# Kernel optimization log

Measured on AMD Instinct MI355X. Metric: run time of the kernel, lower is better.

## Reference

```python
import jax, jax.numpy as jnp
import numpy as np

B, S, HID = 1, 4096, 2048
HQ, HKV, D = 16, 8, 128
G = HQ // HKV
WINDOW = 1024
EPS = 1e-6
ROPE_THETA = 1e6


def setup_inputs() -> dict:
    key = jax.random.key(0)
    ks = jax.random.split(key, 6)
    hidden_states = jax.random.normal(ks[0], (B, S, HID), dtype=jnp.float32)
    Wq = jax.random.normal(ks[1], (HQ * D, HID), dtype=jnp.float32) * 0.02
    Wk = jax.random.normal(ks[2], (HKV * D, HID), dtype=jnp.float32) * 0.02
    Wv = jax.random.normal(ks[3], (HKV * D, HID), dtype=jnp.float32) * 0.02
    Wo = jax.random.normal(ks[4], (HID, HQ * D), dtype=jnp.float32) * 0.02
    q_norm_w = jnp.ones((D,), dtype=jnp.float32)
    k_norm_w = jnp.ones((D,), dtype=jnp.float32)
    # standard RoPE tables
    inv_freq = 1.0 / (ROPE_THETA ** (jnp.arange(0, D, 2, dtype=jnp.float32) / D))
    pos = jnp.arange(S, dtype=jnp.float32)
    freqs = pos[:, None] * inv_freq[None, :]            # [S, D/2]
    emb = jnp.concatenate([freqs, freqs], axis=-1)       # [S, D]
    cos = jnp.cos(emb)[None]                             # [1, S, D]
    sin = jnp.sin(emb)[None]
    return {"hidden_states": hidden_states, "cos": cos, "sin": sin,
            "Wq": Wq, "Wk": Wk, "Wv": Wv, "Wo": Wo,
            "q_norm_w": q_norm_w, "k_norm_w": k_norm_w}


def _rms_norm(x, w):
    var = jnp.mean(jnp.square(x), axis=-1, keepdims=True)
    return w * (x * jax.lax.rsqrt(var + EPS))


def _rotate_half(x):
    x1, x2 = jnp.split(x, 2, axis=-1)
    return jnp.concatenate([-x2, x1], axis=-1)


def reference(hidden_states, cos, sin, Wq, Wk, Wv, Wo, q_norm_w, k_norm_w):
    b, s, _ = hidden_states.shape
    # projections -> [B, H, S, D]
    q = (hidden_states @ Wq.T).reshape(b, s, HQ, D)
    k = (hidden_states @ Wk.T).reshape(b, s, HKV, D)
    v = (hidden_states @ Wv.T).reshape(b, s, HKV, D)
    q = _rms_norm(q, q_norm_w).transpose(0, 2, 1, 3)   # [B,HQ,S,D]
    k = _rms_norm(k, k_norm_w).transpose(0, 2, 1, 3)   # [B,HKV,S,D]
    v = v.transpose(0, 2, 1, 3)
    # RoPE (cos/sin broadcast over head dim)
    c = cos[:, None, :, :]
    sn = sin[:, None, :, :]
    q = q * c + _rotate_half(q) * sn
    k = k * c + _rotate_half(k) * sn
    # GQA: group queries per kv head
    qg = q.reshape(b, HKV, G, s, D)
    scaling = D ** -0.5
    scores = jnp.einsum('bhgqd,bhkd->bhgqk', qg, k) * scaling  # [B,HKV,G,S,S]
    # causal + sliding-window additive mask
    i = jnp.arange(s)[:, None]
    j = jnp.arange(s)[None, :]
    allowed = (j <= i) & (j > i - WINDOW)
    scores = jnp.where(allowed[None, None, None], scores, jnp.float32(-1e9))
    attn = jax.nn.softmax(scores, axis=-1)
    out = jnp.einsum('bhgqk,bhkd->bhgqd', attn, v)     # [B,HKV,G,S,D]
    out = out.reshape(b, HQ, s, D).transpose(0, 2, 1, 3).reshape(b, s, HQ * D)
    return out @ Wo.T
```

## Files before the change

### kernel.cpp

```cpp
#include <hip/hip_runtime.h>

typedef __bf16 bf16;
typedef bf16 bf16x8 __attribute__((ext_vector_type(8)));
typedef bf16 bf16x4 __attribute__((ext_vector_type(4)));
typedef float f32x4 __attribute__((ext_vector_type(4)));

#define MFMA16(a, b, c) __builtin_amdgcn_mfma_f32_16x16x32_bf16((a), (b), (c), 0, 0, 0)

__device__ __forceinline__ void gload_lds16(const bf16* g, bf16* l) {
  __builtin_amdgcn_global_load_lds(
      (const __attribute__((address_space(1))) void*)g,
      (__attribute__((address_space(3))) void*)l, 16, 0, 0);
}

template <int N>
__device__ __forceinline__ void lgkm_fence() {
  if constexpr (N == 0) asm volatile("s_waitcnt lgkmcnt(0)" ::: "memory");
  else if constexpr (N == 4) asm volatile("s_waitcnt lgkmcnt(4)" ::: "memory");
  else if constexpr (N == 8) asm volatile("s_waitcnt lgkmcnt(8)" ::: "memory");
  else if constexpr (N == 12) asm volatile("s_waitcnt lgkmcnt(12)" ::: "memory");
  __builtin_amdgcn_sched_barrier(0);
}
__device__ __forceinline__ void bar_fence() {
  __builtin_amdgcn_sched_barrier(0);
  __builtin_amdgcn_s_barrier();
}

__global__ __launch_bounds__(256) void cvt_f32_bf16(const float* __restrict__ src,
                                                    bf16* __restrict__ dst, int n4) {
  int i = blockIdx.x * blockDim.x + threadIdx.x;
  if (i < n4) {
    float4 v = ((const float4*)src)[i];
    bf16x4 o;
    o[0] = (bf16)v.x; o[1] = (bf16)v.y; o[2] = (bf16)v.z; o[3] = (bf16)v.w;
    ((bf16x4*)dst)[i] = o;
  }
}

template <int BM, int BN, int MT, int NTT, typename OutT>
__global__ __launch_bounds__(512, 2) void gemm_pipe(const bf16* __restrict__ A,
                                                    const bf16* __restrict__ B,
                                                    OutT* __restrict__ C,
                                                    int M, int N, int K) {
  constexpr int MH = MT / 2, NH = NTT / 2;
  constexpr int ASLOT = BM * 64;
  constexpr int BSLOT = BN * 64;
  constexpr int NLA = BM / 64, NLB = BN / 64;
  __shared__ __align__(16) bf16 SA[2 * ASLOT];
  __shared__ __align__(16) bf16 SB[2 * BSLOT];

  const int NTILES = K >> 6;
  const int tid = threadIdx.x;
  const int w = tid >> 6, lane = tid & 63;
  const int l15 = lane & 15, quad = lane >> 4;
  const int wr = w >> 2, wc = w & 3;

  const int nbx = N / BN;
  const int nwg = (M / BM) * nbx;
  const int wg = ((int)blockIdx.x & 7) * (nwg >> 3) + ((int)blockIdx.x >> 3);
  const int bm0 = (wg / nbx) * BM;
  const int bn0 = (wg % nbx) * BN;

  const int r0 = tid >> 3;
  const int sg = (tid & 7) ^ ((tid >> 3) & 7);
  unsigned aoffg[NLA], boffg[NLB];
#pragma unroll
  for (int i = 0; i < NLA; ++i)
    aoffg[i] = (unsigned)((bm0 + r0 + i * 64) * K + sg * 8);
#pragma unroll
  for (int i = 0; i < NLB; ++i)
    boffg[i] = (unsigned)((bn0 + r0 + i * 64) * K + sg * 8);

  const int xl = l15 & 7;
  const int p0 = quad ^ xl;
  const int baseA0 = (wr * (MT * 16) + l15) * 128 + p0 * 16;
  const int baseA1 = (wr * (MT * 16) + l15) * 128 + ((p0 ^ 4) * 16);
  const int baseB0 = (wc * (NTT * 16) + l15) * 128 + p0 * 16;
  const int baseB1 = (wc * (NTT * 16) + l15) * 128 + ((p0 ^ 4) * 16);
  const char* saB = (const char*)&SA[0];
  const char* sbB = (const char*)&SB[0];

  f32x4 acc[MT][NTT] = {};
  bf16x8 As[2][MH][2];
  bf16x8 Bs[2][NH][2];

#define LDA_(SL, H, DST)                                                        \
  _Pragma("unroll") for (int mt = 0; mt < MH; ++mt) {                           \
    (DST)[mt][0] = *(const bf16x8*)(saB + (SL) * (ASLOT * 2) + baseA0 +         \
                                    ((H) * MH + mt) * 2048);                    \
    (DST)[mt][1] = *(const bf16x8*)(saB + (SL) * (ASLOT * 2) + baseA1 +         \
                                    ((H) * MH + mt) * 2048);                    \
  }
#define LDB_(SL, G, DST)                                                        \
  _Pragma("unroll") for (int nt = 0; nt < NH; ++nt) {                           \
    (DST)[nt][0] = *(const bf16x8*)(sbB + (SL) * (BSLOT * 2) + baseB0 +         \
                                    ((G) * NH + nt) * 2048);                    \
    (DST)[nt][1] = *(const bf16x8*)(sbB + (SL) * (BSLOT * 2) + baseB1 +         \
                                    ((G) * NH + nt) * 2048);                    \
  }
#define QMFMA_(AS, BS, MHI, NHI)                                                \
  __builtin_amdgcn_s_setprio(1);                                                \
  _Pragma("unroll") for (int mt = 0; mt < MH; ++mt)                             \
      _Pragma("unroll") for (int nt = 0; nt < NH; ++nt) {                       \
    acc[(MHI) * MH + mt][(NHI) * NH + nt] = MFMA16(                             \
        (AS)[mt][0], (BS)[nt][0], acc[(MHI) * MH + mt][(NHI) * NH + nt]);       \
    acc[(MHI) * MH + mt][(NHI) * NH + nt] = MFMA16(                             \
        (AS)[mt][1], (BS)[nt][1], acc[(MHI) * MH + mt][(NHI) * NH + nt]);       \
  }                                                                             \
  __builtin_amdgcn_s_setprio(0);
#define STAGE_(SO, TS)                                                          \
  _Pragma("unroll") for (int i = 0; i < NLA; ++i)                               \
      gload_lds16(A + aoffg[i] + (TS) * 64, SA + (SO) * ASLOT + tid * 8 + i * 4096); \
  _Pragma("unroll") for (int i = 0; i < NLB; ++i)                               \
      gload_lds16(B + boffg[i] + (TS) * 64, SB + (SO) * BSLOT + tid * 8 + i * 4096);

#define GTILE_BODY(PAR, TS)                                                     \
  {                                                                             \
    constexpr int sl_ = (PAR), so_ = (PAR) ^ 1;                                 \
    constexpr int e0_ = (PAR), e1_ = (PAR) ^ 1;                                 \
                                                                        \
    LDB_(sl_, 1, Bs[e1_]);                                                      \
    bar_fence();                                                                \
    lgkm_fence<NTT>();                                                          \
    if ((TS) < NTILES) { STAGE_(so_, (TS)); }                                   \
    QMFMA_(As[0], Bs[e0_], 0, 0);                                               \
                                                                        \
    LDA_(sl_, 1, As[1]);                                                        \
    bar_fence();                                                                \
    lgkm_fence<MT>();                                                           \
    QMFMA_(As[0], Bs[e1_], 0, 1);                                               \
                                                                        \
    LDB_(sl_, 0, Bs[e0_]);                                                      \
    asm volatile("s_waitcnt vmcnt(0)" ::: "memory");                            \
    bar_fence();                                                                \
    lgkm_fence<NTT>();                                                          \
    QMFMA_(As[1], Bs[e1_], 1, 1);                                               \
                                                                        \
    LDA_(so_, 0, As[0]);                                                        \
    LDB_(so_, 0, Bs[e1_]);                                                      \
    bar_fence();                                                                \
    lgkm_fence<MT + NTT>();                                                     \
    QMFMA_(As[1], Bs[e0_], 1, 0);                                               \
  }

  { STAGE_(0, 0); }
  asm volatile("s_waitcnt vmcnt(0)" ::: "memory");
  bar_fence();
  __builtin_amdgcn_sched_barrier(0);
  LDA_(0, 0, As[0]);
  LDB_(0, 0, Bs[0]);

  for (int t = 0; t < NTILES; t += 2) {
    GTILE_BODY(0, t + 1);
    GTILE_BODY(1, t + 2);
  }

#undef LDA_
#undef LDB_
#undef QMFMA_
#undef STAGE_
#undef GTILE_BODY

#pragma unroll
  for (int mt = 0; mt < MT; ++mt)
#pragma unroll
    for (int nt = 0; nt < NTT; ++nt) {
      int row = bm0 + wr * (MT * 16) + mt * 16 + quad * 4;
      int col = bn0 + wc * (NTT * 16) + nt * 16 + l15;
#pragma unroll
      for (int r = 0; r < 4; ++r)
        C[(size_t)(row + r) * N + col] = (OutT)acc[mt][nt][r];
    }
}

__global__ __launch_bounds__(256) void normrope(const bf16* __restrict__ QKVb,
                                                const float* __restrict__ cosb,
                                                const float* __restrict__ sinb,
                                                const float* __restrict__ qw,
                                                const float* __restrict__ kw,
                                                bf16* __restrict__ Qb,
                                                bf16* __restrict__ Kb) {
  const int wid = (blockIdx.x * blockDim.x + threadIdx.x) >> 6;
  const int lane = threadIdx.x & 63;
  const int s = wid / 24;
  const int h = wid % 24;
  const bool isq = (h < 16);
  const int col0 = isq ? h * 128 : 2048 + (h - 16) * 128;
  const float* wt = isq ? qw : kw;

  const bf16* row = QKVb + (size_t)s * 4096 + col0;
  float x1 = (float)row[lane];
  float x2 = (float)row[lane + 64];

  float ss = x1 * x1 + x2 * x2;
#pragma unroll
  for (int m = 32; m >= 1; m >>= 1) ss += __shfl_xor(ss, m, 64);
  float rs = rsqrtf(ss * (1.0f / 128.0f) + 1e-6f);

  float c = cosb[(size_t)s * 128 + lane];
  float sn = sinb[(size_t)s * 128 + lane];
  float xn1 = x1 * rs * wt[lane];
  float xn2 = x2 * rs * wt[lane + 64];
  float o1 = xn1 * c - xn2 * sn;
  float o2 = xn2 * c + xn1 * sn;
  const float scale = isq ? 0.12751652f : 1.0f;
  o1 *= scale; o2 *= scale;

  bf16* dst = isq ? (Qb + ((size_t)h * 4096 + s) * 128)
                  : (Kb + ((size_t)(h - 16) * 4096 + s) * 128);
  dst[lane] = (bf16)o1;
  dst[lane + 64] = (bf16)o2;
}

__global__ __launch_bounds__(256) void vtrans(const bf16* __restrict__ QKVb,
                                              bf16* __restrict__ Vtp) {
  __shared__ __align__(16) bf16 T[64 * 136];
  const int kvh = blockIdx.y;
  const int s0 = blockIdx.x * 64;
  const int tid = threadIdx.x;
  for (int g = tid; g < 1024; g += 256) {
    int s = g >> 4, cg = g & 15;
    *(bf16x8*)(T + s * 136 + cg * 8) =
        *(const bf16x8*)(QKVb + (size_t)(s0 + s) * 4096 + 3072 + kvh * 128 + cg * 8);
  }
  __syncthreads();
  for (int g = tid; g < 1024; g += 256) {
    int d = g >> 3, sg = g & 7;
    bf16x8 v;
#pragma unroll
    for (int j = 0; j < 8; j++) {
      int kp = sg * 8 + j;
      int s = (kp & 3) * 16 + (kp >> 2);
      v[j] = T[s * 136 + d];
    }
    *(bf16x8*)(Vtp + ((size_t)kvh * 128 + d) * 4096 + s0 + sg * 8) = v;
  }
}

__global__ __launch_bounds__(512, 1) void attn_kernel(const bf16* __restrict__ Qb,
                                                      const bf16* __restrict__ Kb,
                                                      const bf16* __restrict__ Vtp,
                                                      bf16* __restrict__ Ob) {
  const int SEQ = 4096, W = 1024;
  const float MP = 17.312340f;
  __shared__ __align__(16) bf16 Ks[2][64 * 128];
  __shared__ __align__(16) bf16 Vs[2][128 * 64];
  __shared__ __align__(16) bf16 Ps[8][32 * 64];

  const int id = blockIdx.x;
  const int kvh = id & 7, gq = (id >> 3) & 1, h = kvh * 2 + gq;
  const int qb0 = (id >> 4) * 256;
  const int tid = threadIdx.x, w = tid >> 6, lane = tid & 63;
  const int l15 = lane & 15, quad = lane >> 4;
  const int qw0 = qb0 + w * 32;

  bf16x8 qf[2][4];
#pragma unroll
  for (int m = 0; m < 2; m++) {
    const bf16* qp = Qb + ((size_t)h * SEQ + qw0 + m * 16 + l15) * 128 + quad * 8;
#pragma unroll
    for (int kb = 0; kb < 4; kb++) qf[m][kb] = *(const bf16x8*)(qp + kb * 32);
  }

  f32x4 o[2][8] = {};
  f32x4 lr[2] = {};
  bf16* pw = &Ps[w][0];
  const bf16* kbase = Kb + (size_t)kvh * SEQ * 128;
  const bf16* vbase = Vtp + (size_t)kvh * 128 * SEQ;

  int jmin = qb0 - (W - 1); if (jmin < 0) jmin = 0;
  const int kt0 = jmin >> 6, kt1 = (qb0 + 255) >> 6;

#define ASTAGE(KT, SL)                                                          \
  do {                                                                          \
    const int k0_ = (KT) * 64;                                                  \
    _Pragma("unroll") for (int i_ = 0; i_ < 2; ++i_) {                          \
      int slot = i_ * 512 + tid;                                                \
      int key = slot >> 4, gg = slot & 15;                                      \
      int gsw = gg ^ (key & 7);                                                 \
      gload_lds16(kbase + (size_t)(k0_ + key) * 128 + gsw * 8,                  \
                  &Ks[SL][0] + slot * 8);                                       \
    }                                                                           \
    _Pragma("unroll") for (int i_ = 0; i_ < 2; ++i_) {                          \
      int slot = i_ * 512 + tid;                                                \
      int d = slot >> 3, gg = slot & 7;                                         \
      int gsw = gg ^ (d & 7);                                                   \
      gload_lds16(vbase + (size_t)d * SEQ + k0_ + gsw * 8,                      \
                  &Vs[SL][0] + slot * 8);                                       \
    }                                                                           \
  } while (0)

  ASTAGE(kt0, 0);

  for (int kt = kt0; kt <= kt1; ++kt) {
    const int sl = (kt - kt0) & 1;
    if (kt < kt1) {
      ASTAGE(kt + 1, sl ^ 1);
      asm volatile("s_waitcnt vmcnt(4)" ::: "memory");
    } else {
      asm volatile("s_waitcnt vmcnt(0)" ::: "memory");
    }
    __builtin_amdgcn_s_barrier();

    const int k0 = kt * 64;
    const bf16* ks = &Ks[sl][0];
    const bf16* vs = &Vs[sl][0];
    const bool alive = (k0 <= qw0 + 31) && (k0 + 63 > qw0 - W);
    if (alive) {
      const bool full = (k0 + 63 <= qw0) && (k0 > qw0 + 31 - W);
      f32x4 s[2][4] = {};
#pragma unroll
      for (int c = 0; c < 4; c++) {
        const int key = c * 16 + l15;
        bf16x8 kf[4];
#pragma unroll
        for (int kb = 0; kb < 4; kb++)
          kf[kb] = *(const bf16x8*)(ks + key * 128 + (((kb * 4 + quad) ^ (key & 7)) << 3));
        __builtin_amdgcn_s_setprio(1);
#pragma unroll
        for (int kb = 0; kb < 4; kb++) {
          s[0][c] = MFMA16(qf[0][kb], kf[kb], s[0][c]);
          s[1][c] = MFMA16(qf[1][kb], kf[kb], s[1][c]);
        }
        __builtin_amdgcn_s_setprio(0);
      }
#pragma unroll
      for (int m = 0; m < 2; m++)
#pragma unroll
        for (int r = 0; r < 4; r++) {
          float p[4];
          if (full) {
#pragma unroll
            for (int c = 0; c < 4; c++) p[c] = __builtin_amdgcn_exp2f(s[m][c][r] - MP);
          } else {
            const int i_ = qw0 + m * 16 + quad * 4 + r;
#pragma unroll
            for (int c = 0; c < 4; c++) {
              int j = k0 + c * 16 + l15;
              p[c] = (j <= i_ && j > i_ - W) ? __builtin_amdgcn_exp2f(s[m][c][r] - MP) : 0.0f;
            }
          }
          lr[m][r] += p[0] + p[1] + p[2] + p[3];
          bf16x4 pk;
          pk[0] = (bf16)p[0]; pk[1] = (bf16)p[1]; pk[2] = (bf16)p[2]; pk[3] = (bf16)p[3];
          const int qrow = m * 16 + quad * 4 + r;
          *(bf16x4*)(pw + qrow * 64 + (((l15 >> 1) ^ (qrow & 7)) << 3) + (l15 & 1) * 4) = pk;
        }
      asm volatile("s_waitcnt lgkmcnt(0)" ::: "memory");
      bf16x8 pf[2][2];
#pragma unroll
      for (int m = 0; m < 2; m++)
#pragma unroll
        for (int kb = 0; kb < 2; kb++)
          pf[m][kb] = *(const bf16x8*)(pw + (m * 16 + l15) * 64 +
                                       (((kb * 4 + quad) ^ (l15 & 7)) << 3));
#pragma unroll
      for (int n = 0; n < 8; n++) {
        const int d = n * 16 + l15;
        bf16x8 vf0 = *(const bf16x8*)(vs + d * 64 + ((quad ^ (l15 & 7)) << 3));
        bf16x8 vf1 = *(const bf16x8*)(vs + d * 64 + (((4 + quad) ^ (l15 & 7)) << 3));
        __builtin_amdgcn_s_setprio(1);
        o[0][n] = MFMA16(pf[0][0], vf0, o[0][n]);
        o[0][n] = MFMA16(pf[0][1], vf1, o[0][n]);
        o[1][n] = MFMA16(pf[1][0], vf0, o[1][n]);
        o[1][n] = MFMA16(pf[1][1], vf1, o[1][n]);
        __builtin_amdgcn_s_setprio(0);
      }
    }
    __builtin_amdgcn_s_barrier();
  }
#undef ASTAGE

  float linv[2][4];
#pragma unroll
  for (int m = 0; m < 2; m++)
#pragma unroll
    for (int r = 0; r < 4; r++) {
      float v = lr[m][r];
      v += __shfl_xor(v, 1, 64);
      v += __shfl_xor(v, 2, 64);
      v += __shfl_xor(v, 4, 64);
      v += __shfl_xor(v, 8, 64);
      linv[m][r] = 1.0f / v;
    }
#pragma unroll
  for (int m = 0; m < 2; m++)
#pragma unroll
    for (int n = 0; n < 8; n++)
#pragma unroll
      for (int r = 0; r < 4; r++) {
        int i_ = qw0 + m * 16 + quad * 4 + r;
        Ob[(size_t)i_ * 2048 + h * 128 + n * 16 + l15] = (bf16)(o[m][n][r] * linv[m][r]);
      }
}

extern "C" void kernel_launch(void* const* d_in, const int* in_sizes, int n_in,
                              void* d_out, int out_size, void* d_ws, size_t ws_size,
                              hipStream_t stream) {
  const float* hid  = (const float*)d_in[0];
  const float* cosb = (const float*)d_in[1];
  const float* sinb = (const float*)d_in[2];
  const float* Wq   = (const float*)d_in[3];
  const float* Wk   = (const float*)d_in[4];
  const float* Wv   = (const float*)d_in[5];
  const float* Wo   = (const float*)d_in[6];
  const float* qw   = (const float*)d_in[7];
  const float* kw   = (const float*)d_in[8];

  if (ws_size < (size_t)(112u) * 1024u * 1024u) return;

  char* ws = (char*)d_ws;
  bf16* Xbf  = (bf16*)(ws);
  bf16* Vtp  = (bf16*)(ws);
  bf16* Wcat = (bf16*)(ws + (16u << 20));
  bf16* Wob  = (bf16*)(ws + (32u << 20));
  bf16* QKVb = (bf16*)(ws + (40u << 20));
  bf16* Qb   = (bf16*)(ws + (72u << 20));
  bf16* Kb   = (bf16*)(ws + (88u << 20));
  bf16* Ob   = (bf16*)(ws + (96u << 20));

  cvt_f32_bf16<<<8192, 256, 0, stream>>>(hid, Xbf, 2097152);
  cvt_f32_bf16<<<4096, 256, 0, stream>>>(Wq, Wcat, 1048576);
  cvt_f32_bf16<<<2048, 256, 0, stream>>>(Wk, Wcat + 4194304, 524288);
  cvt_f32_bf16<<<2048, 256, 0, stream>>>(Wv, Wcat + 6291456, 524288);
  cvt_f32_bf16<<<4096, 256, 0, stream>>>(Wo, Wob, 1048576);

  gemm_pipe<256, 256, 8, 4, bf16><<<256, 512, 0, stream>>>(Xbf, Wcat, QKVb, 4096, 4096, 2048);
  vtrans<<<dim3(64, 8), 256, 0, stream>>>(QKVb, Vtp);
  normrope<<<24576, 256, 0, stream>>>(QKVb, cosb, sinb, qw, kw, Qb, Kb);
  attn_kernel<<<256, 512, 0, stream>>>(Qb, Kb, Vtp, Ob);
  gemm_pipe<128, 256, 4, 4, float><<<256, 512, 0, stream>>>(Ob, Wob, (float*)d_out, 4096, 2048, 2048);
}
```

Before: 329.5 us.

## Merge conversion and prep launches; split-K the output projection with a reduction pass

Five f32-to-bf16 conversion launches become one, and the V-transpose and norm/RoPE kernels are merged into a single launch to cut launch overhead. The output projection now uses 256x256 tiles with a two-way K split, writing two f32 partials into workspace that a separate add kernel sums into the output. This trades fewer tiles per CU and less reuse for larger tiles, at the cost of an extra 32MB partial write/read pass and one more launch.

```diff
diff --git a/kernel.cpp b/kernel.cpp
--- a/kernel.cpp
+++ b/kernel.cpp
@@ -26,21 +26,42 @@
   __builtin_amdgcn_s_barrier();
 }
 
-__global__ __launch_bounds__(256) void cvt_f32_bf16(const float* __restrict__ src,
-                                                    bf16* __restrict__ dst, int n4) {
-  int i = blockIdx.x * blockDim.x + threadIdx.x;
-  if (i < n4) {
-    float4 v = ((const float4*)src)[i];
-    bf16x4 o;
-    o[0] = (bf16)v.x; o[1] = (bf16)v.y; o[2] = (bf16)v.z; o[3] = (bf16)v.w;
-    ((bf16x4*)dst)[i] = o;
-  }
-}
-
-template <int BM, int BN, int MT, int NTT, typename OutT>
+__global__ __launch_bounds__(256) void cvt_all(const float* __restrict__ hid,
+                                               const float* __restrict__ wq,
+                                               const float* __restrict__ wk,
+                                               const float* __restrict__ wv,
+                                               const float* __restrict__ wo,
+                                               bf16* __restrict__ xbf,
+                                               bf16* __restrict__ wcat,
+                                               bf16* __restrict__ wob) {
+  int j = blockIdx.x * 256 + threadIdx.x;
+  const float* src;
+  bf16* dst;
+  if (j < 2097152) { src = hid; dst = xbf; }
+  else {
+    j -= 2097152;
+    if (j < 1048576) { src = wq; dst = wcat; }
+    else {
+      j -= 1048576;
+      if (j < 524288) { src = wk; dst = wcat + 4194304; }
+      else {
+        j -= 524288;
+        if (j < 524288) { src = wv; dst = wcat + 6291456; }
+        else { j -= 524288; src = wo; dst = wob; }
+      }
+    }
+  }
+  float4 v = ((const float4*)src)[j];
+  bf16x4 o;
+  o[0] = (bf16)v.x; o[1] = (bf16)v.y; o[2] = (bf16)v.z; o[3] = (bf16)v.w;
+  ((bf16x4*)dst)[j] = o;
+}
+
+template <int BM, int BN, int MT, int NTT, int NSPLIT, typename OutT>
 __global__ __launch_bounds__(512, 2) void gemm_pipe(const bf16* __restrict__ A,
                                                     const bf16* __restrict__ B,
-                                                    OutT* __restrict__ C,
+                                                    OutT* __restrict__ C0,
+                                                    OutT* __restrict__ C1,
                                                     int M, int N, int K) {
   constexpr int MH = MT / 2, NH = NTT / 2;
   constexpr int ASLOT = BM * 64;
@@ -49,7 +70,6 @@
   __shared__ __align__(16) bf16 SA[2 * ASLOT];
   __shared__ __align__(16) bf16 SB[2 * BSLOT];
 
-  const int NTILES = K >> 6;
   const int tid = threadIdx.x;
   const int w = tid >> 6, lane = tid & 63;
   const int l15 = lane & 15, quad = lane >> 4;
@@ -57,7 +77,16 @@
 
   const int nbx = N / BN;
   const int nwg = (M / BM) * nbx;
-  const int wg = ((int)blockIdx.x & 7) * (nwg >> 3) + ((int)blockIdx.x >> 3);
+  int bx = (int)blockIdx.x;
+  int split = 0;
+  if constexpr (NSPLIT > 1) { split = bx / nwg; bx -= split * nwg; }
+  const int Keff = K / NSPLIT;
+  const int NTILES = Keff >> 6;
+  OutT* __restrict__ C = (split ? C1 : C0);
+  const bf16* __restrict__ Ab = A + (size_t)split * Keff;
+  const bf16* __restrict__ Bb = B + (size_t)split * Keff;
+
+  const int wg = (bx & 7) * (nwg >> 3) + (bx >> 3);
   const int bm0 = (wg / nbx) * BM;
   const int bn0 = (wg % nbx) * BN;
 
@@ -110,9 +139,9 @@
   __builtin_amdgcn_s_setprio(0);
 #define STAGE_(SO, TS)                                                          \
   _Pragma("unroll") for (int i = 0; i < NLA; ++i)                               \
-      gload_lds16(A + aoffg[i] + (TS) * 64, SA + (SO) * ASLOT + tid * 8 + i * 4096); \
+      gload_lds16(Ab + aoffg[i] + (TS) * 64, SA + (SO) * ASLOT + tid * 8 + i * 4096); \
   _Pragma("unroll") for (int i = 0; i < NLB; ++i)                               \
-      gload_lds16(B + boffg[i] + (TS) * 64, SB + (SO) * BSLOT + tid * 8 + i * 4096);
+      gload_lds16(Bb + boffg[i] + (TS) * 64, SB + (SO) * BSLOT + tid * 8 + i * 4096);
 
 #define GTILE_BODY(PAR, TS)                                                     \
   {                                                                             \
@@ -173,67 +202,80 @@
     }
 }
 
-__global__ __launch_bounds__(256) void normrope(const bf16* __restrict__ QKVb,
-                                                const float* __restrict__ cosb,
-                                                const float* __restrict__ sinb,
-                                                const float* __restrict__ qw,
-                                                const float* __restrict__ kw,
-                                                bf16* __restrict__ Qb,
-                                                bf16* __restrict__ Kb) {
-  const int wid = (blockIdx.x * blockDim.x + threadIdx.x) >> 6;
-  const int lane = threadIdx.x & 63;
-  const int s = wid / 24;
-  const int h = wid % 24;
-  const bool isq = (h < 16);
-  const int col0 = isq ? h * 128 : 2048 + (h - 16) * 128;
-  const float* wt = isq ? qw : kw;
-
-  const bf16* row = QKVb + (size_t)s * 4096 + col0;
-  float x1 = (float)row[lane];
-  float x2 = (float)row[lane + 64];
-
-  float ss = x1 * x1 + x2 * x2;
-#pragma unroll
-  for (int m = 32; m >= 1; m >>= 1) ss += __shfl_xor(ss, m, 64);
-  float rs = rsqrtf(ss * (1.0f / 128.0f) + 1e-6f);
-
-  float c = cosb[(size_t)s * 128 + lane];
-  float sn = sinb[(size_t)s * 128 + lane];
-  float xn1 = x1 * rs * wt[lane];
-  float xn2 = x2 * rs * wt[lane + 64];
-  float o1 = xn1 * c - xn2 * sn;
-  float o2 = xn2 * c + xn1 * sn;
-  const float scale = isq ? 0.12751652f : 1.0f;
-  o1 *= scale; o2 *= scale;
-
-  bf16* dst = isq ? (Qb + ((size_t)h * 4096 + s) * 128)
-                  : (Kb + ((size_t)(h - 16) * 4096 + s) * 128);
-  dst[lane] = (bf16)o1;
-  dst[lane + 64] = (bf16)o2;
-}
-
-__global__ __launch_bounds__(256) void vtrans(const bf16* __restrict__ QKVb,
-                                              bf16* __restrict__ Vtp) {
+__global__ __launch_bounds__(256) void addred(const float4* __restrict__ p0,
+                                              const float4* __restrict__ p1,
+                                              float4* __restrict__ out, int n4) {
+  int i = blockIdx.x * 256 + threadIdx.x;
+  if (i < n4) {
+    float4 a = p0[i], b = p1[i];
+    float4 o;
+    o.x = a.x + b.x; o.y = a.y + b.y; o.z = a.z + b.z; o.w = a.w + b.w;
+    out[i] = o;
+  }
+}
+
+__global__ __launch_bounds__(256) void prep(const bf16* __restrict__ QKVb,
+                                            const float* __restrict__ cosb,
+                                            const float* __restrict__ sinb,
+                                            const float* __restrict__ qw,
+                                            const float* __restrict__ kw,
+                                            bf16* __restrict__ Qb,
+                                            bf16* __restrict__ Kb,
+                                            bf16* __restrict__ Vtp) {
   __shared__ __align__(16) bf16 T[64 * 136];
-  const int kvh = blockIdx.y;
-  const int s0 = blockIdx.x * 64;
+  const int b = blockIdx.x;
   const int tid = threadIdx.x;
-  for (int g = tid; g < 1024; g += 256) {
-    int s = g >> 4, cg = g & 15;
-    *(bf16x8*)(T + s * 136 + cg * 8) =
-        *(const bf16x8*)(QKVb + (size_t)(s0 + s) * 4096 + 3072 + kvh * 128 + cg * 8);
-  }
-  __syncthreads();
-  for (int g = tid; g < 1024; g += 256) {
-    int d = g >> 3, sg = g & 7;
-    bf16x8 v;
-#pragma unroll
-    for (int j = 0; j < 8; j++) {
-      int kp = sg * 8 + j;
-      int s = (kp & 3) * 16 + (kp >> 2);
-      v[j] = T[s * 136 + d];
-    }
-    *(bf16x8*)(Vtp + ((size_t)kvh * 128 + d) * 4096 + s0 + sg * 8) = v;
+  if (b < 512) {
+    const int kvh = b >> 6;
+    const int s0 = (b & 63) * 64;
+    for (int g = tid; g < 1024; g += 256) {
+      int s = g >> 4, cg = g & 15;
+      *(bf16x8*)(T + s * 136 + cg * 8) =
+          *(const bf16x8*)(QKVb + (size_t)(s0 + s) * 4096 + 3072 + kvh * 128 + cg * 8);
+    }
+    __syncthreads();
+    for (int g = tid; g < 1024; g += 256) {
+      int d = g >> 3, sg = g & 7;
+      bf16x8 v;
+#pragma unroll
+      for (int j = 0; j < 8; j++) {
+        int kp = sg * 8 + j;
+        int s = (kp & 3) * 16 + (kp >> 2);
+        v[j] = T[s * 136 + d];
+      }
+      *(bf16x8*)(Vtp + ((size_t)kvh * 128 + d) * 4096 + s0 + sg * 8) = v;
+    }
+  } else {
+    const int wid = ((b - 512) * 256 + tid) >> 6;
+    const int lane = tid & 63;
+    const int s = wid / 24;
+    const int h = wid % 24;
+    const bool isq = (h < 16);
+    const int col0 = isq ? h * 128 : 2048 + (h - 16) * 128;
+    const float* wt = isq ? qw : kw;
+
+    const bf16* row = QKVb + (size_t)s * 4096 + col0;
+    float x1 = (float)row[lane];
+    float x2 = (float)row[lane + 64];
+
+    float ss = x1 * x1 + x2 * x2;
+#pragma unroll
+    for (int m = 32; m >= 1; m >>= 1) ss += __shfl_xor(ss, m, 64);
+    float rs = rsqrtf(ss * (1.0f / 128.0f) + 1e-6f);
+
+    float c = cosb[(size_t)s * 128 + lane];
+    float sn = sinb[(size_t)s * 128 + lane];
+    float xn1 = x1 * rs * wt[lane];
+    float xn2 = x2 * rs * wt[lane + 64];
+    float o1 = xn1 * c - xn2 * sn;
+    float o2 = xn2 * c + xn1 * sn;
+    const float scale = isq ? 0.12751652f : 1.0f;
+    o1 *= scale; o2 *= scale;
+
+    bf16* dst = isq ? (Qb + ((size_t)h * 4096 + s) * 128)
+                    : (Kb + ((size_t)(h - 16) * 4096 + s) * 128);
+    dst[lane] = (bf16)o1;
+    dst[lane + 64] = (bf16)o2;
   }
 }
 
@@ -412,22 +454,26 @@
   char* ws = (char*)d_ws;
   bf16* Xbf  = (bf16*)(ws);
   bf16* Vtp  = (bf16*)(ws);
+  float* P1  = (float*)(ws);
   bf16* Wcat = (bf16*)(ws + (16u << 20));
   bf16* Wob  = (bf16*)(ws + (32u << 20));
   bf16* QKVb = (bf16*)(ws + (40u << 20));
+  float* P0  = (float*)(ws + (40u << 20));
   bf16* Qb   = (bf16*)(ws + (72u << 20));
   bf16* Kb   = (bf16*)(ws + (88u << 20));
   bf16* Ob   = (bf16*)(ws + (96u << 20));
 
-  cvt_f32_bf16<<<8192, 256, 0, stream>>>(hid, Xbf, 2097152);
-  cvt_f32_bf16<<<4096, 256, 0, stream>>>(Wq, Wcat, 1048576);
-  cvt_f32_bf16<<<2048, 256, 0, stream>>>(Wk, Wcat + 4194304, 524288);
-  cvt_f32_bf16<<<2048, 256, 0, stream>>>(Wv, Wcat + 6291456, 524288);
-  cvt_f32_bf16<<<4096, 256, 0, stream>>>(Wo, Wob, 1048576);
-
-  gemm_pipe<256, 256, 8, 4, bf16><<<256, 512, 0, stream>>>(Xbf, Wcat, QKVb, 4096, 4096, 2048);
-  vtrans<<<dim3(64, 8), 256, 0, stream>>>(QKVb, Vtp);
-  normrope<<<24576, 256, 0, stream>>>(QKVb, cosb, sinb, qw, kw, Qb, Kb);
+  cvt_all<<<20480, 256, 0, stream>>>(hid, Wq, Wk, Wv, Wo, Xbf, Wcat, Wob);
+
+  gemm_pipe<256, 256, 8, 4, 1, bf16><<<256, 512, 0, stream>>>(
+      Xbf, Wcat, QKVb, QKVb, 4096, 4096, 2048);
+
+  prep<<<25088, 256, 0, stream>>>(QKVb, cosb, sinb, qw, kw, Qb, Kb, Vtp);
+
   attn_kernel<<<256, 512, 0, stream>>>(Qb, Kb, Vtp, Ob);
-  gemm_pipe<128, 256, 4, 4, float><<<256, 512, 0, stream>>>(Ob, Wob, (float*)d_out, 4096, 2048, 2048);
-}
+
+  gemm_pipe<256, 256, 8, 4, 2, float><<<256, 512, 0, stream>>>(
+      Ob, Wob, P0, P1, 4096, 2048, 2048);
+  addred<<<8192, 256, 0, stream>>>((const float4*)P0, (const float4*)P1,
+                                   (float4*)d_out, 2097152);
+}
```

Result: no change. 329.8 us (+0.1%).
